# Kernel tuning notes

Measured on AMD Instinct MI355X. Metric: run time of the kernel, lower is better.

The kernel has to match this reference:

```python
import jax, jax.numpy as jnp
import numpy as np

N = 50000
E = 800000
DIN = 256
DH = 256
DOUT = 256
R = 8
B = 4


def setup_inputs() -> dict:
    key = jax.random.key(0)
    ks = jax.random.split(key, 12)
    s = 0.05
    return {
        "x": jax.random.normal(ks[0], (N, DIN), jnp.float32),
        "edge_index": jax.random.randint(ks[1], (2, E), 0, N, jnp.int64),
        "edge_type": jax.random.randint(ks[2], (E,), 0, R, jnp.int64),
        "basis1": jax.random.normal(ks[3], (B, DIN, DH), jnp.float32) * s,
        "comp1": jax.random.normal(ks[4], (R, B), jnp.float32) * s,
        "root1": jax.random.normal(ks[5], (DIN, DH), jnp.float32) * s,
        "bias1": jnp.zeros((DH,), jnp.float32),
        "basis2": jax.random.normal(ks[6], (B, DH, DOUT), jnp.float32) * s,
        "comp2": jax.random.normal(ks[7], (R, B), jnp.float32) * s,
        "root2": jax.random.normal(ks[8], (DH, DOUT), jnp.float32) * s,
        "bias2": jnp.zeros((DOUT,), jnp.float32),
    }


def rgcn_conv(x, src, dst, edge_type, basis, comp, root, bias):
    # Basis-decomposed relational conv (PyG RGCNConv, aggr='mean').
    # xb: per-node transform by each basis matrix -> [N, B, out]
    xb = jnp.einsum('ni,bio->nbo', x, basis)
    # Per-edge message: mix bases with relation coefficients -> [E, out]
    msg = jnp.einsum('eb,ebo->eo', comp[edge_type], xb[src])
    # Mean aggregation per (dst, relation): divide each edge by the count of
    # edges of its relation arriving at its destination, then scatter-add.
    key = dst * R + edge_type
    cnt = jax.ops.segment_sum(jnp.ones((msg.shape[0],), x.dtype), key,
                              num_segments=x.shape[0] * R)
    norm = 1.0 / jnp.maximum(cnt, 1.0)
    agg = jax.ops.segment_sum(msg * norm[key][:, None], dst,
                              num_segments=x.shape[0])
    return agg + x @ root + bias


def reference(x, edge_index, edge_type, basis1, comp1, root1, bias1,
              basis2, comp2, root2, bias2):
    src, dst = edge_index[0], edge_index[1]
    h = rgcn_conv(x, src, dst, edge_type, basis1, comp1, root1, bias1)
    h = jax.nn.relu(h)
    # dropout(p=0.4) is identity in eval mode
    out = rgcn_conv(h, src, dst, edge_type, basis2, comp2, root2, bias2)
    return out
```

## Files before the change

### kernel.cpp

```cpp
#include <hip/hip_runtime.h>
#include <hip/hip_bf16.h>

constexpr int N_NODES = 50000;
constexpr int N_EDGES = 800000;
constexpr int R_REL   = 8;
constexpr int BASES   = 4;
constexpr int D       = 256;
constexpr int KZ      = BASES * D;
constexpr int KT      = KZ + D;

typedef __attribute__((ext_vector_type(8))) short bf16x8;
typedef __attribute__((ext_vector_type(4))) float f32x4;

__device__ inline float bfu_lo(unsigned u) { return __uint_as_float(u << 16); }
__device__ inline float bfu_hi(unsigned u) { return __uint_as_float(u & 0xFFFF0000u); }
__device__ inline unsigned short f2bu(float f) {
  __hip_bfloat16 h = __float2bfloat16(f);
  return *reinterpret_cast<unsigned short*>(&h);
}
__device__ inline void store_out(float* p, float v) { *p = v; }
__device__ inline void store_out(__hip_bfloat16* p, float v) { *p = __float2bfloat16(v); }

__device__ inline void gload_lds16(void* lds, const void* g) {
  __builtin_amdgcn_global_load_lds(
      (const __attribute__((address_space(1))) unsigned*)g,
      (__attribute__((address_space(3))) unsigned*)lds, 16, 0, 0);
}

__global__ __launch_bounds__(256) void count_kernel(
    const int* __restrict__ ei, const int* __restrict__ et,
    int* __restrict__ cnt) {
  int e = blockIdx.x * 256 + threadIdx.x;
  if (e < N_EDGES) {
    int dst = ei[N_EDGES + e];
    int rt  = et[e];
    atomicAdd(&cnt[dst * R_REL + rt], 1);
  }
}

__global__ __launch_bounds__(256) void scan_phaseA(
    const int* __restrict__ cnt, int* __restrict__ bsum) {
  __shared__ int sd[256];
  int tid = threadIdx.x;
  int n = blockIdx.x * 256 + tid;
  int d = 0;
  if (n < N_NODES) {
#pragma unroll
    for (int r = 0; r < R_REL; r++) d += cnt[n * R_REL + r];
  }
  sd[tid] = d;
  __syncthreads();
  for (int off = 128; off > 0; off >>= 1) {
    if (tid < off) sd[tid] += sd[tid + off];
    __syncthreads();
  }
  if (tid == 0) bsum[blockIdx.x] = sd[0];
}

__global__ __launch_bounds__(256) void scan_phaseB(
    const int* __restrict__ bsum, int* __restrict__ boff,
    int* __restrict__ estart, int NB) {
  __shared__ int sd[256];
  int tid = threadIdx.x;
  int v = (tid < NB) ? bsum[tid] : 0;
  sd[tid] = v;
  __syncthreads();
  for (int off = 1; off < 256; off <<= 1) {
    int t = (tid >= off) ? sd[tid - off] : 0;
    __syncthreads();
    sd[tid] += t;
    __syncthreads();
  }
  if (tid < NB) boff[tid] = sd[tid] - v;
  if (tid == 0) estart[N_NODES] = N_EDGES;
}

__global__ __launch_bounds__(256) void scan_phaseC(
    const int* __restrict__ cnt, const int* __restrict__ boff,
    int* __restrict__ estart) {
  __shared__ int sd[256];
  int tid = threadIdx.x;
  int n = blockIdx.x * 256 + tid;
  int d = 0;
  if (n < N_NODES) {
#pragma unroll
    for (int r = 0; r < R_REL; r++) d += cnt[n * R_REL + r];
  }
  sd[tid] = d;
  __syncthreads();
  for (int off = 1; off < 256; off <<= 1) {
    int t = (tid >= off) ? sd[tid - off] : 0;
    __syncthreads();
    sd[tid] += t;
    __syncthreads();
  }
  if (n < N_NODES) estart[n] = boff[blockIdx.x] + sd[tid] - d;
}

__global__ __launch_bounds__(256) void bucket_kernel(
    const int* __restrict__ ei, const int* __restrict__ et,
    const int* __restrict__ estart, int* __restrict__ cursor,
    int* __restrict__ packed) {
  int e = blockIdx.x * 256 + threadIdx.x;
  if (e < N_EDGES) {
    int src = ei[e];
    int dst = ei[N_EDGES + e];
    int rt  = et[e];
    int pos = estart[dst] + atomicAdd(&cursor[dst], 1);
    packed[pos] = src | (rt << 20);
  }
}

__global__ __launch_bounds__(256) void convert_kernel(
    const float* __restrict__ x, unsigned* __restrict__ x2) {
  int idx = blockIdx.x * 256 + threadIdx.x;
  if (idx < N_NODES * 128) {
    float2 v = *(const float2*)(x + (size_t)idx * 2);
    x2[idx] = (unsigned)f2bu(v.x) | ((unsigned)f2bu(v.y) << 16);
  }
}

__global__ __launch_bounds__(256) void winv_kernel(
    const int* __restrict__ cnt, const float* __restrict__ comp,
    float4* __restrict__ wtab) {
  int idx = blockIdx.x * 256 + threadIdx.x;
  if (idx < N_NODES * R_REL) {
    int r = idx & 7;
    int c = cnt[idx];
    float inv = 1.0f / (float)(c > 0 ? c : 1);
    float4 w;
    w.x = comp[r * BASES + 0] * inv;
    w.y = comp[r * BASES + 1] * inv;
    w.z = comp[r * BASES + 2] * inv;
    w.w = comp[r * BASES + 3] * inv;
    wtab[idx] = w;
  }
}

__global__ __launch_bounds__(256) void make_w_kernel(
    const float* __restrict__ basis, const float* __restrict__ root,
    __hip_bfloat16* __restrict__ WT) {
  __shared__ __hip_bfloat16 tile[64][256];
  int k0 = blockIdx.x * 64;
  int tid = threadIdx.x;
#pragma unroll 4
  for (int r = 0; r < 64; r++) {
    int k = k0 + r;
    const float* srow = (k < KZ)
        ? basis + ((size_t)(k & 3) * D + (k >> 2)) * D
        : root + (size_t)(k - KZ) * D;
    tile[r][tid] = __float2bfloat16(srow[tid]);
  }
  __syncthreads();
  __hip_bfloat16* dst = WT + (size_t)tid * KT + k0;
#pragma unroll
  for (int c = 0; c < 8; c++) {
    union { short s[8]; int4 v; } u;
#pragma unroll
    for (int r = 0; r < 8; r++)
      u.s[r] = *reinterpret_cast<short*>(&tile[c * 8 + r][tid]);
    *(int4*)(dst + c * 8) = u.v;
  }
}

__device__ inline float2 pfma(float s, float2 a, float2 c) {
  c.x = fmaf(s, a.x, c.x);
  c.y = fmaf(s, a.y, c.y);
  return c;
}

__device__ inline void edge_fma(float2 acc[BASES][2], uint2 v, float4 w) {
  float2 a01 = make_float2(bfu_lo(v.x), bfu_hi(v.x));
  float2 a23 = make_float2(bfu_lo(v.y), bfu_hi(v.y));
  acc[0][0] = pfma(w.x, a01, acc[0][0]); acc[0][1] = pfma(w.x, a23, acc[0][1]);
  acc[1][0] = pfma(w.y, a01, acc[1][0]); acc[1][1] = pfma(w.y, a23, acc[1][1]);
  acc[2][0] = pfma(w.z, a01, acc[2][0]); acc[2][1] = pfma(w.z, a23, acc[2][1]);
  acc[3][0] = pfma(w.w, a01, acc[3][0]); acc[3][1] = pfma(w.w, a23, acc[3][1]);
}

__global__ __launch_bounds__(256) void aggregate_kernel(
    const unsigned* __restrict__ x2,
    const int* __restrict__ packed,
    const int* __restrict__ estart,
    const float4* __restrict__ wtab,
    __hip_bfloat16* __restrict__ zA)
{
  int tid = threadIdx.x;
  int wave = tid >> 6, lane = tid & 63;
  int n = blockIdx.x * 4 + wave;
  const float4 wzero = make_float4(0.f, 0.f, 0.f, 0.f);

  float2 acc[BASES][2] = {};
  int s = estart[n], e = estart[n + 1];
  const float4* wt = wtab + (size_t)n * R_REL;

  for (int base = s; base < e; base += 8) {
    int rem = e - base;
    int p[8];
#pragma unroll
    for (int k = 0; k < 8; k++)
      p[k] = packed[base + (rem > k ? k : 0)];
    uint2 v[8];
#pragma unroll
    for (int k = 0; k < 8; k++)
      v[k] = *(const uint2*)(x2 + (size_t)(p[k] & 0xFFFFF) * 128 + lane * 2);
    float4 w[8];
#pragma unroll
    for (int k = 0; k < 8; k++)
      w[k] = (rem > k) ? wt[p[k] >> 20] : wzero;
#pragma unroll
    for (int k = 0; k < 8; k++)
      edge_fma(acc, v[k], w[k]);
  }

  union { short s[8]; int4 v; } u0, u1;
#pragma unroll
  for (int b = 0; b < BASES; b++) {
    u0.s[b]     = (short)f2bu(acc[b][0].x);
    u0.s[4 + b] = (short)f2bu(acc[b][0].y);
    u1.s[b]     = (short)f2bu(acc[b][1].x);
    u1.s[4 + b] = (short)f2bu(acc[b][1].y);
  }
  __hip_bfloat16* zrow = zA + (size_t)n * KZ;
  *(int4*)(zrow + 16 * lane) = u0.v;
  *(int4*)(zrow + 16 * lane + 8) = u1.v;
}

#define BM 128
#define BN 256
#define BK 32

template <bool RELU, typename OutT>
__global__ __launch_bounds__(512) void gemm_kernel(
    const __hip_bfloat16* __restrict__ Az,
    const __hip_bfloat16* __restrict__ Aself,
    const __hip_bfloat16* __restrict__ Bt,
    const float* __restrict__ bias, OutT* __restrict__ C, int M) {
  __shared__ __align__(16) __hip_bfloat16 As[BM * BK];
  __shared__ __align__(16) __hip_bfloat16 Bs[BN * BK];
  int tid = threadIdx.x;
  int m0 = blockIdx.x * BM;
  int wave = tid >> 6, lane = tid & 63;
  int wm = wave & 1, wn = wave >> 1;
  int l15 = lane & 15, quad = lane >> 4;

  int colS = (lane & 3) * 8;
  int rowA = wave * 16 + (lane >> 2);
  int grA  = min(m0 + rowA, M - 1);
  const __hip_bfloat16* gAz = Az + (size_t)grA * KZ + colS;
  const __hip_bfloat16* gAs = Aself + (size_t)grA * D + colS;
  const __hip_bfloat16* gB0 = Bt + (size_t)(wave * 32 + (lane >> 2)) * KT + colS;
  const __hip_bfloat16* gB1 = gB0 + 16 * KT;
  __hip_bfloat16* lA  = As + wave * 512;
  __hip_bfloat16* lB0 = Bs + wave * 1024;
  __hip_bfloat16* lB1 = Bs + wave * 1024 + 512;

  f32x4 acc[4][4] = {};

  for (int k0 = 0; k0 < KT; k0 += BK) {
    const __hip_bfloat16* srcA = (k0 < KZ) ? (gAz + k0) : (gAs + (k0 - KZ));
    gload_lds16(lA, srcA);
    gload_lds16(lB0, gB0 + k0);
    gload_lds16(lB1, gB1 + k0);
    __syncthreads();

    bf16x8 af[4], bfr[4];
#pragma unroll
    for (int mt = 0; mt < 4; mt++)
      af[mt] = *(const bf16x8*)(As + (wm * 64 + mt * 16 + l15) * BK + quad * 8);
#pragma unroll
    for (int nt = 0; nt < 4; nt++)
      bfr[nt] = *(const bf16x8*)(Bs + (wn * 64 + nt * 16 + l15) * BK + quad * 8);
#pragma unroll
    for (int mt = 0; mt < 4; mt++)
#pragma unroll
      for (int nt = 0; nt < 4; nt++)
        acc[mt][nt] = __builtin_amdgcn_mfma_f32_16x16x32_bf16(
            af[mt], bfr[nt], acc[mt][nt], 0, 0, 0);
    __syncthreads();
  }

#pragma unroll
  for (int nt = 0; nt < 4; nt++) {
    int cg = wn * 64 + nt * 16 + l15;
    float bv = bias[cg];
#pragma unroll
    for (int mt = 0; mt < 4; mt++) {
#pragma unroll
      for (int r = 0; r < 4; r++) {
        int rg = m0 + wm * 64 + mt * 16 + quad * 4 + r;
        if (rg < M) {
          float v = acc[mt][nt][r] + bv;
          if (RELU) v = fmaxf(v, 0.f);
          store_out(C + (size_t)rg * D + cg, v);
        }
      }
    }
  }
}

static inline char* carve(char*& p, size_t bytes) {
  char* r = p;
  p += (bytes + 255) & ~(size_t)255;
  return r;
}

extern "C" void kernel_launch(void* const* d_in, const int* in_sizes, int n_in,
                              void* d_out, int out_size, void* d_ws,
                              size_t ws_size, hipStream_t stream) {
  const float* x      = (const float*)d_in[0];
  const int*   ei     = (const int*)d_in[1];
  const int*   et     = (const int*)d_in[2];
  const float* basis1 = (const float*)d_in[3];
  const float* comp1  = (const float*)d_in[4];
  const float* root1  = (const float*)d_in[5];
  const float* bias1  = (const float*)d_in[6];
  const float* basis2 = (const float*)d_in[7];
  const float* comp2  = (const float*)d_in[8];
  const float* root2  = (const float*)d_in[9];
  const float* bias2  = (const float*)d_in[10];
  float* out = (float*)d_out;

  char* ws = (char*)d_ws;
  int* cnt    = (int*)carve(ws, (size_t)N_NODES * R_REL * 4);
  int* estart = (int*)carve(ws, (size_t)(N_NODES + 1) * 4);
  int* cursor = (int*)carve(ws, (size_t)N_NODES * 4);
  int* bsum   = (int*)carve(ws, 256 * 4);
  int* boff   = (int*)carve(ws, 256 * 4);
  int* packed = (int*)carve(ws, (size_t)N_EDGES * 4);
  float4* wtab1 = (float4*)carve(ws, (size_t)N_NODES * R_REL * 16);
  float4* wtab2 = (float4*)carve(ws, (size_t)N_NODES * R_REL * 16);
  __hip_bfloat16* WT1 = (__hip_bfloat16*)carve(ws, (size_t)D * KT * 2);
  __hip_bfloat16* WT2 = (__hip_bfloat16*)carve(ws, (size_t)D * KT * 2);
  unsigned* xb = (unsigned*)carve(ws, (size_t)N_NODES * D * 2);
  __hip_bfloat16* h = (__hip_bfloat16*)carve(ws, (size_t)N_NODES * D * 2);
  __hip_bfloat16* zA = (__hip_bfloat16*)carve(ws, (size_t)N_NODES * KZ * 2);

  const int NB = (N_NODES + 255) / 256;
  const int EB = (N_EDGES + 255) / 256;
  const int CB = (N_NODES * 128 + 255) / 256;
  const int WB = (N_NODES * R_REL + 255) / 256;

  hipMemsetAsync(cnt, 0, (size_t)N_NODES * R_REL * 4, stream);
  hipMemsetAsync(cursor, 0, (size_t)N_NODES * 4, stream);

  count_kernel<<<EB, 256, 0, stream>>>(ei, et, cnt);
  scan_phaseA<<<NB, 256, 0, stream>>>(cnt, bsum);
  scan_phaseB<<<1, 256, 0, stream>>>(bsum, boff, estart, NB);
  scan_phaseC<<<NB, 256, 0, stream>>>(cnt, boff, estart);
  bucket_kernel<<<EB, 256, 0, stream>>>(ei, et, estart, cursor, packed);

  convert_kernel<<<CB, 256, 0, stream>>>(x, xb);
  winv_kernel<<<WB, 256, 0, stream>>>(cnt, comp1, wtab1);
  winv_kernel<<<WB, 256, 0, stream>>>(cnt, comp2, wtab2);
  make_w_kernel<<<KT / 64, 256, 0, stream>>>(basis1, root1, WT1);
  make_w_kernel<<<KT / 64, 256, 0, stream>>>(basis2, root2, WT2);

  dim3 ggrid((N_NODES + BM - 1) / BM, 1);
  const int AB = (N_NODES + 3) / 4;

  aggregate_kernel<<<AB, 256, 0, stream>>>(xb, packed, estart, wtab1, zA);
  gemm_kernel<true, __hip_bfloat16><<<ggrid, 512, 0, stream>>>(
      zA, (const __hip_bfloat16*)xb, WT1, bias1, h, N_NODES);

  aggregate_kernel<<<AB, 256, 0, stream>>>((const unsigned*)h, packed, estart,
                                           wtab2, zA);
  gemm_kernel<false, float><<<ggrid, 512, 0, stream>>>(
      zA, h, WT2, bias2, out, N_NODES);
}
```

Before: 491.3 us.

## Pad CSR segments to multiples of eight and fuse preprocessing kernels

Each node's edge list is padded to a multiple of eight with a dummy entry that points to relation slot 8, and that slot in a widened 16-entry weight table holds zeros. This lets the aggregation loop drop its per-edge bounds checks and read the packed indices with vector loads into scalar registers via readfirstlane. Several small preprocessing launches (count, convert, weight transpose, padding fill, scan phase A plus weight-table build, cursor reset) are merged into fewer kernels to cut launch overhead. The cost is extra padded edges that load real row 0 data and multiply it by zero weights, plus larger packed and weight-table buffers.

```diff
diff --git a/kernel.cpp b/kernel.cpp
--- a/kernel.cpp
+++ b/kernel.cpp
@@ -8,6 +8,16 @@
 constexpr int D       = 256;
 constexpr int KZ      = BASES * D;
 constexpr int KT      = KZ + D;
+constexpr int WSTRIDE = 16;
+constexpr int DUMMY_P = 8 << 20;
+
+constexpr int EB  = (N_EDGES + 255) / 256;
+constexpr int NB  = (N_NODES + 255) / 256;
+constexpr int CB  = (N_NODES * 128) / 256;
+constexpr int WKB = KT / 64;
+constexpr int WB  = (N_NODES * WSTRIDE) / 256;
+constexpr int CAP = N_EDGES + N_NODES * 8;
+constexpr int FB  = (CAP + 255) / 256;
 
 typedef __attribute__((ext_vector_type(8))) short bf16x8;
 typedef __attribute__((ext_vector_type(4))) float f32x4;
@@ -27,39 +37,116 @@
       (__attribute__((address_space(3))) unsigned*)lds, 16, 0, 0);
 }
 
-__global__ __launch_bounds__(256) void count_kernel(
+__global__ __launch_bounds__(256) void prep_kernel(
     const int* __restrict__ ei, const int* __restrict__ et,
-    int* __restrict__ cnt) {
-  int e = blockIdx.x * 256 + threadIdx.x;
-  if (e < N_EDGES) {
-    int dst = ei[N_EDGES + e];
-    int rt  = et[e];
-    atomicAdd(&cnt[dst * R_REL + rt], 1);
-  }
-}
-
-__global__ __launch_bounds__(256) void scan_phaseA(
-    const int* __restrict__ cnt, int* __restrict__ bsum) {
+    int* __restrict__ cnt,
+    const float* __restrict__ x, unsigned* __restrict__ x2,
+    const float* __restrict__ basis1, const float* __restrict__ root1,
+    __hip_bfloat16* __restrict__ WT1,
+    const float* __restrict__ basis2, const float* __restrict__ root2,
+    __hip_bfloat16* __restrict__ WT2,
+    int* __restrict__ packed) {
+  __shared__ __hip_bfloat16 tile[64][256];
+  int bid = blockIdx.x;
+  int tid = threadIdx.x;
+
+  if (bid < EB) {
+    int e = bid * 256 + tid;
+    if (e < N_EDGES) {
+      int dst = ei[N_EDGES + e];
+      atomicAdd(&cnt[dst * R_REL + et[e]], 1);
+    }
+    return;
+  }
+  bid -= EB;
+  if (bid < CB) {
+    int idx = bid * 256 + tid;
+    float2 v = *(const float2*)(x + (size_t)idx * 2);
+    x2[idx] = (unsigned)f2bu(v.x) | ((unsigned)f2bu(v.y) << 16);
+    return;
+  }
+  bid -= CB;
+  if (bid < 2 * WKB) {
+    const float* basis = (bid < WKB) ? basis1 : basis2;
+    const float* root  = (bid < WKB) ? root1 : root2;
+    __hip_bfloat16* WT = (bid < WKB) ? WT1 : WT2;
+    int wb = (bid < WKB) ? bid : bid - WKB;
+    int k0 = wb * 64;
+#pragma unroll 4
+    for (int r = 0; r < 64; r++) {
+      int k = k0 + r;
+      const float* srow = (k < KZ)
+          ? basis + ((size_t)(k & 3) * D + (k >> 2)) * D
+          : root + (size_t)(k - KZ) * D;
+      tile[r][tid] = __float2bfloat16(srow[tid]);
+    }
+    __syncthreads();
+    __hip_bfloat16* dst = WT + (size_t)tid * KT + k0;
+#pragma unroll
+    for (int c = 0; c < 8; c++) {
+      union { short s[8]; int4 v; } u;
+#pragma unroll
+      for (int r = 0; r < 8; r++)
+        u.s[r] = *reinterpret_cast<short*>(&tile[c * 8 + r][tid]);
+      *(int4*)(dst + c * 8) = u.v;
+    }
+    return;
+  }
+  bid -= 2 * WKB;
+  {
+    int i = bid * 256 + tid;
+    if (i < CAP) packed[i] = DUMMY_P;
+  }
+}
+
+__global__ __launch_bounds__(256) void scanA_winv_kernel(
+    const int* __restrict__ cnt, int* __restrict__ bsum,
+    const float* __restrict__ comp1, float4* __restrict__ wtab1,
+    const float* __restrict__ comp2, float4* __restrict__ wtab2) {
   __shared__ int sd[256];
-  int tid = threadIdx.x;
-  int n = blockIdx.x * 256 + tid;
-  int d = 0;
-  if (n < N_NODES) {
-#pragma unroll
-    for (int r = 0; r < R_REL; r++) d += cnt[n * R_REL + r];
-  }
-  sd[tid] = d;
-  __syncthreads();
-  for (int off = 128; off > 0; off >>= 1) {
-    if (tid < off) sd[tid] += sd[tid + off];
-    __syncthreads();
-  }
-  if (tid == 0) bsum[blockIdx.x] = sd[0];
+  int bid = blockIdx.x;
+  int tid = threadIdx.x;
+  if (bid < NB) {
+    int n = bid * 256 + tid;
+    int d = 0;
+    if (n < N_NODES) {
+#pragma unroll
+      for (int r = 0; r < R_REL; r++) d += cnt[n * R_REL + r];
+      d = (d + 7) & ~7;
+    }
+    sd[tid] = d;
+    __syncthreads();
+    for (int off = 128; off > 0; off >>= 1) {
+      if (tid < off) sd[tid] += sd[tid + off];
+      __syncthreads();
+    }
+    if (tid == 0) bsum[bid] = sd[0];
+    return;
+  }
+  bid -= NB;
+  {
+    const float* comp = (bid < WB) ? comp1 : comp2;
+    float4* wtab = (bid < WB) ? wtab1 : wtab2;
+    int lb = (bid < WB) ? bid : bid - WB;
+    int idx = lb * 256 + tid;
+    int r = idx & (WSTRIDE - 1);
+    int n = idx >> 4;
+    float4 w = make_float4(0.f, 0.f, 0.f, 0.f);
+    if (r < R_REL) {
+      int c = cnt[n * R_REL + r];
+      float inv = 1.0f / (float)(c > 0 ? c : 1);
+      w.x = comp[r * BASES + 0] * inv;
+      w.y = comp[r * BASES + 1] * inv;
+      w.z = comp[r * BASES + 2] * inv;
+      w.w = comp[r * BASES + 3] * inv;
+    }
+    wtab[idx] = w;
+  }
 }
 
 __global__ __launch_bounds__(256) void scan_phaseB(
     const int* __restrict__ bsum, int* __restrict__ boff,
-    int* __restrict__ estart, int NB) {
+    int* __restrict__ estart) {
   __shared__ int sd[256];
   int tid = threadIdx.x;
   int v = (tid < NB) ? bsum[tid] : 0;
@@ -72,12 +159,12 @@
     __syncthreads();
   }
   if (tid < NB) boff[tid] = sd[tid] - v;
-  if (tid == 0) estart[N_NODES] = N_EDGES;
+  if (tid == NB - 1) estart[N_NODES] = sd[tid];
 }
 
 __global__ __launch_bounds__(256) void scan_phaseC(
     const int* __restrict__ cnt, const int* __restrict__ boff,
-    int* __restrict__ estart) {
+    int* __restrict__ estart, int* __restrict__ cursor) {
   __shared__ int sd[256];
   int tid = threadIdx.x;
   int n = blockIdx.x * 256 + tid;
@@ -85,6 +172,7 @@
   if (n < N_NODES) {
 #pragma unroll
     for (int r = 0; r < R_REL; r++) d += cnt[n * R_REL + r];
+    d = (d + 7) & ~7;
   }
   sd[tid] = d;
   __syncthreads();
@@ -94,7 +182,10 @@
     sd[tid] += t;
     __syncthreads();
   }
-  if (n < N_NODES) estart[n] = boff[blockIdx.x] + sd[tid] - d;
+  if (n < N_NODES) {
+    estart[n] = boff[blockIdx.x] + sd[tid] - d;
+    cursor[n] = 0;
+  }
 }
 
 __global__ __launch_bounds__(256) void bucket_kernel(
@@ -111,58 +202,6 @@
   }
 }
 
-__global__ __launch_bounds__(256) void convert_kernel(
-    const float* __restrict__ x, unsigned* __restrict__ x2) {
-  int idx = blockIdx.x * 256 + threadIdx.x;
-  if (idx < N_NODES * 128) {
-    float2 v = *(const float2*)(x + (size_t)idx * 2);
-    x2[idx] = (unsigned)f2bu(v.x) | ((unsigned)f2bu(v.y) << 16);
-  }
-}
-
-__global__ __launch_bounds__(256) void winv_kernel(
-    const int* __restrict__ cnt, const float* __restrict__ comp,
-    float4* __restrict__ wtab) {
-  int idx = blockIdx.x * 256 + threadIdx.x;
-  if (idx < N_NODES * R_REL) {
-    int r = idx & 7;
-    int c = cnt[idx];
-    float inv = 1.0f / (float)(c > 0 ? c : 1);
-    float4 w;
-    w.x = comp[r * BASES + 0] * inv;
-    w.y = comp[r * BASES + 1] * inv;
-    w.z = comp[r * BASES + 2] * inv;
-    w.w = comp[r * BASES + 3] * inv;
-    wtab[idx] = w;
-  }
-}
-
-__global__ __launch_bounds__(256) void make_w_kernel(
-    const float* __restrict__ basis, const float* __restrict__ root,
-    __hip_bfloat16* __restrict__ WT) {
-  __shared__ __hip_bfloat16 tile[64][256];
-  int k0 = blockIdx.x * 64;
-  int tid = threadIdx.x;
-#pragma unroll 4
-  for (int r = 0; r < 64; r++) {
-    int k = k0 + r;
-    const float* srow = (k < KZ)
-        ? basis + ((size_t)(k & 3) * D + (k >> 2)) * D
-        : root + (size_t)(k - KZ) * D;
-    tile[r][tid] = __float2bfloat16(srow[tid]);
-  }
-  __syncthreads();
-  __hip_bfloat16* dst = WT + (size_t)tid * KT + k0;
-#pragma unroll
-  for (int c = 0; c < 8; c++) {
-    union { short s[8]; int4 v; } u;
-#pragma unroll
-    for (int r = 0; r < 8; r++)
-      u.s[r] = *reinterpret_cast<short*>(&tile[c * 8 + r][tid]);
-    *(int4*)(dst + c * 8) = u.v;
-  }
-}
-
 __device__ inline float2 pfma(float s, float2 a, float2 c) {
   c.x = fmaf(s, a.x, c.x);
   c.y = fmaf(s, a.y, c.y);
@@ -186,31 +225,58 @@
     __hip_bfloat16* __restrict__ zA)
 {
   int tid = threadIdx.x;
-  int wave = tid >> 6, lane = tid & 63;
-  int n = blockIdx.x * 4 + wave;
-  const float4 wzero = make_float4(0.f, 0.f, 0.f, 0.f);
+  int lane = tid & 63;
+  int n = __builtin_amdgcn_readfirstlane(blockIdx.x * 4 + (tid >> 6));
+  int s = __builtin_amdgcn_readfirstlane(estart[n]);
+  int e = __builtin_amdgcn_readfirstlane(estart[n + 1]);
+  const int voff = lane * 2;
+  const float4* wt = wtab + (size_t)n * WSTRIDE;
 
   float2 acc[BASES][2] = {};
-  int s = estart[n], e = estart[n + 1];
-  const float4* wt = wtab + (size_t)n * R_REL;
 
   for (int base = s; base < e; base += 8) {
-    int rem = e - base;
-    int p[8];
-#pragma unroll
-    for (int k = 0; k < 8; k++)
-      p[k] = packed[base + (rem > k ? k : 0)];
-    uint2 v[8];
-#pragma unroll
-    for (int k = 0; k < 8; k++)
-      v[k] = *(const uint2*)(x2 + (size_t)(p[k] & 0xFFFFF) * 128 + lane * 2);
-    float4 w[8];
-#pragma unroll
-    for (int k = 0; k < 8; k++)
-      w[k] = (rem > k) ? wt[p[k] >> 20] : wzero;
-#pragma unroll
-    for (int k = 0; k < 8; k++)
-      edge_fma(acc, v[k], w[k]);
+    int4 q0 = *(const int4*)(packed + base);
+    int4 q1 = *(const int4*)(packed + base + 4);
+    int p0 = __builtin_amdgcn_readfirstlane(q0.x);
+    int p1 = __builtin_amdgcn_readfirstlane(q0.y);
+    int p2 = __builtin_amdgcn_readfirstlane(q0.z);
+    int p3 = __builtin_amdgcn_readfirstlane(q0.w);
+    int p4 = __builtin_amdgcn_readfirstlane(q1.x);
+    int p5 = __builtin_amdgcn_readfirstlane(q1.y);
+    int p6 = __builtin_amdgcn_readfirstlane(q1.z);
+    int p7 = __builtin_amdgcn_readfirstlane(q1.w);
+    const unsigned* r0 = x2 + ((size_t)(p0 & 0xFFFFF) << 7);
+    const unsigned* r1 = x2 + ((size_t)(p1 & 0xFFFFF) << 7);
+    const unsigned* r2 = x2 + ((size_t)(p2 & 0xFFFFF) << 7);
+    const unsigned* r3 = x2 + ((size_t)(p3 & 0xFFFFF) << 7);
+    const unsigned* r4 = x2 + ((size_t)(p4 & 0xFFFFF) << 7);
+    const unsigned* r5 = x2 + ((size_t)(p5 & 0xFFFFF) << 7);
+    const unsigned* r6 = x2 + ((size_t)(p6 & 0xFFFFF) << 7);
+    const unsigned* r7 = x2 + ((size_t)(p7 & 0xFFFFF) << 7);
+    uint2 v0 = *(const uint2*)(r0 + voff);
+    uint2 v1 = *(const uint2*)(r1 + voff);
+    uint2 v2 = *(const uint2*)(r2 + voff);
+    uint2 v3 = *(const uint2*)(r3 + voff);
+    uint2 v4 = *(const uint2*)(r4 + voff);
+    uint2 v5 = *(const uint2*)(r5 + voff);
+    uint2 v6 = *(const uint2*)(r6 + voff);
+    uint2 v7 = *(const uint2*)(r7 + voff);
+    float4 w0 = wt[p0 >> 20];
+    float4 w1 = wt[p1 >> 20];
+    float4 w2 = wt[p2 >> 20];
+    float4 w3 = wt[p3 >> 20];
+    float4 w4 = wt[p4 >> 20];
+    float4 w5 = wt[p5 >> 20];
+    float4 w6 = wt[p6 >> 20];
+    float4 w7 = wt[p7 >> 20];
+    edge_fma(acc, v0, w0);
+    edge_fma(acc, v1, w1);
+    edge_fma(acc, v2, w2);
+    edge_fma(acc, v3, w3);
+    edge_fma(acc, v4, w4);
+    edge_fma(acc, v5, w5);
+    edge_fma(acc, v6, w6);
+    edge_fma(acc, v7, w7);
   }
 
   union { short s[8]; int4 v; } u0, u1;
@@ -327,34 +393,24 @@
   int* cursor = (int*)carve(ws, (size_t)N_NODES * 4);
   int* bsum   = (int*)carve(ws, 256 * 4);
   int* boff   = (int*)carve(ws, 256 * 4);
-  int* packed = (int*)carve(ws, (size_t)N_EDGES * 4);
-  float4* wtab1 = (float4*)carve(ws, (size_t)N_NODES * R_REL * 16);
-  float4* wtab2 = (float4*)carve(ws, (size_t)N_NODES * R_REL * 16);
+  int* packed = (int*)carve(ws, (size_t)CAP * 4);
+  float4* wtab1 = (float4*)carve(ws, (size_t)N_NODES * WSTRIDE * 16);
+  float4* wtab2 = (float4*)carve(ws, (size_t)N_NODES * WSTRIDE * 16);
   __hip_bfloat16* WT1 = (__hip_bfloat16*)carve(ws, (size_t)D * KT * 2);
   __hip_bfloat16* WT2 = (__hip_bfloat16*)carve(ws, (size_t)D * KT * 2);
   unsigned* xb = (unsigned*)carve(ws, (size_t)N_NODES * D * 2);
   __hip_bfloat16* h = (__hip_bfloat16*)carve(ws, (size_t)N_NODES * D * 2);
   __hip_bfloat16* zA = (__hip_bfloat16*)carve(ws, (size_t)N_NODES * KZ * 2);
 
-  const int NB = (N_NODES + 255) / 256;
-  const int EB = (N_EDGES + 255) / 256;
-  const int CB = (N_NODES * 128 + 255) / 256;
-  const int WB = (N_NODES * R_REL + 255) / 256;
-
   hipMemsetAsync(cnt, 0, (size_t)N_NODES * R_REL * 4, stream);
-  hipMemsetAsync(cursor, 0, (size_t)N_NODES * 4, stream);
-
-  count_kernel<<<EB, 256, 0, stream>>>(ei, et, cnt);
-  scan_phaseA<<<NB, 256, 0, stream>>>(cnt, bsum);
-  scan_phaseB<<<1, 256, 0, stream>>>(bsum, boff, estart, NB);
-  scan_phaseC<<<NB, 256, 0, stream>>>(cnt, boff, estart);
+
+  prep_kernel<<<EB + CB + 2 * WKB + FB, 256, 0, stream>>>(
+      ei, et, cnt, x, xb, basis1, root1, WT1, basis2, root2, WT2, packed);
+  scanA_winv_kernel<<<NB + 2 * WB, 256, 0, stream>>>(cnt, bsum, comp1, wtab1,
+                                                     comp2, wtab2);
+  scan_phaseB<<<1, 256, 0, stream>>>(bsum, boff, estart);
+  scan_phaseC<<<NB, 256, 0, stream>>>(cnt, boff, estart, cursor);
   bucket_kernel<<<EB, 256, 0, stream>>>(ei, et, estart, cursor, packed);
-
-  convert_kernel<<<CB, 256, 0, stream>>>(x, xb);
-  winv_kernel<<<WB, 256, 0, stream>>>(cnt, comp1, wtab1);
-  winv_kernel<<<WB, 256, 0, stream>>>(cnt, comp2, wtab2);
-  make_w_kernel<<<KT / 64, 256, 0, stream>>>(basis1, root1, WT1);
-  make_w_kernel<<<KT / 64, 256, 0, stream>>>(basis2, root2, WT2);
 
   dim3 ggrid((N_NODES + BM - 1) / BM, 1);
   const int AB = (N_NODES + 3) / 4;
```

After: 468.4 us. 1.05x faster.
